# Performance work log

Hardware: AMD Instinct MI355X
Metric: run time of the kernel (lower is better)

Reference implementation:

```python
import jax, jax.numpy as jnp
import numpy as np

B, S, H = 2, 2048, 1024
E, K, F = 64, 8, 512
NORM_TOPK = True
CAP_FACTOR = 2.0


def setup_inputs() -> dict:
    key = jax.random.key(0)
    k0, k1, k2, k3, k4 = jax.random.split(key, 5)
    s_h = 1.0 / np.sqrt(H)
    s_f = 1.0 / np.sqrt(F)
    return {
        "hidden_states": jax.random.normal(k0, (B, S, H), jnp.float32),
        "w_gate": jax.random.normal(k1, (H, E), jnp.float32) * s_h,  # gate: Linear(H->E), no bias
        "w1": jax.random.normal(k2, (E, H, F), jnp.float32) * s_h,   # gate_proj per expert
        "w3": jax.random.normal(k3, (E, H, F), jnp.float32) * s_h,   # up_proj per expert
        "w2": jax.random.normal(k4, (E, F, H), jnp.float32) * s_f,   # down_proj per expert
    }


def reference(hidden_states, w_gate, w1, w3, w2):
    b, s, h = hidden_states.shape
    e = w_gate.shape[1]
    t = b * s
    x = hidden_states.reshape(t, h)
    router_logits = x @ w_gate                                   # [T, E]
    probs = jax.nn.softmax(router_logits.astype(jnp.float32), axis=-1)
    topw, sel = jax.lax.top_k(probs, K)                          # [T, K]
    if NORM_TOPK:
        topw = topw / jnp.sum(topw, axis=-1, keepdims=True)
    topw = topw.astype(x.dtype)

    a = t * K                                                    # total assignments
    c = int(CAP_FACTOR * a / e)                                  # static per-expert capacity
    sel_flat = sel.reshape(a)
    w_flat = topw.reshape(a)
    tok = jnp.repeat(jnp.arange(t), K)
    order = jnp.argsort(sel_flat, stable=True)                   # group assignments by expert
    e_s, t_s, w_s = sel_flat[order], tok[order], w_flat[order]
    counts = jnp.bincount(sel_flat, length=e)
    starts = jnp.cumsum(counts) - counts
    pos = jnp.arange(a) - starts[e_s]                            # position within expert group
    valid = pos < c
    slot = jnp.where(valid, e_s * c + pos, e * c)                # overflow -> dropped sentinel slot

    # dispatch: gather tokens into per-expert contiguous buffer [E, C, H]
    buf = jnp.zeros((e * c + 1, h), x.dtype).at[slot].set(x[t_s])
    xb = buf[: e * c].reshape(e, c, h)
    # grouped gated-SiLU MLP per expert
    g = jnp.einsum('ech,ehf->ecf', xb, w1)
    u = jnp.einsum('ech,ehf->ecf', xb, w3)
    yb = jnp.einsum('ecf,efh->ech', jax.nn.silu(g) * u, w2).reshape(e * c, h)
    # combine: weighted scatter-add back to tokens
    contrib = yb[jnp.minimum(slot, e * c - 1)] * (w_s * valid.astype(x.dtype))[:, None]
    out = jnp.zeros((t, h), x.dtype).at[t_s].add(contrib)
    return out.reshape(b, s, h), router_logits
```

## Files before the change

### kernel.cpp

```cpp
#include <hip/hip_runtime.h>
#include <hip/hip_bf16.h>

#define T_TOK 4096
#define H_DIM 1024
#define E_EXP 64
#define TOPK  8
#define F_DIM 512
#define CAP   1024
#define A_TOT (T_TOK * TOPK)

typedef _Float16 f16;
typedef _Float16 f16x4 __attribute__((ext_vector_type(4)));
typedef _Float16 f16x8 __attribute__((ext_vector_type(8)));
typedef float    f32x4 __attribute__((ext_vector_type(4)));

__global__ __launch_bounds__(256) void pack_all_kernel(
    const float* __restrict__ w1, const float* __restrict__ w3,
    const float* __restrict__ w2,
    f16* __restrict__ w1p, f16* __restrict__ w3p, f16* __restrict__ w2p)
{
    __shared__ f16 Ls[32][516];
    const int tid = threadIdx.x;
    const int bid = blockIdx.x;
    const float* src; f16* dst; int Nd, kb, e, kt, ch;
    if (bid < 2048)      { src = w1; dst = w1p; Nd = 512;  kb = 32; e = bid >> 5;          kt = bid & 31;          ch = 0; }
    else if (bid < 4096) { src = w3; dst = w3p; Nd = 512;  kb = 32; e = (bid - 2048) >> 5; kt = (bid - 2048) & 31; ch = 0; }
    else { src = w2; dst = w2p; Nd = 1024; kb = 16; int r = bid - 4096; e = r >> 5; kt = (r >> 1) & 15; ch = r & 1; }
    const int Kd = kb << 5;

    const float* base = src + ((size_t)e * Kd + kt * 32) * Nd + ch * 512;
    #pragma unroll
    for (int p = 0; p < 16; ++p) {
        int idx = p * 256 + tid;
        int row = idx >> 7, c4 = (idx & 127) * 4;
        float4 v = *(const float4*)(base + (size_t)row * Nd + c4);
        f16x4 hv;
        hv[0] = (f16)v.x; hv[1] = (f16)v.y; hv[2] = (f16)v.z; hv[3] = (f16)v.w;
        *(f16x4*)&Ls[row][c4] = hv;
    }
    __syncthreads();
    const int lane = tid & 63, wvi = tid >> 6;
    const int jj = lane & 15, qq = lane >> 4;
    const int ntb = Nd >> 4;
    #pragma unroll
    for (int i = 0; i < 8; ++i) {
        int ntl = wvi * 8 + i;
        f16x8 o;
        #pragma unroll
        for (int j = 0; j < 8; ++j)
            o[j] = Ls[qq * 8 + j][ntl * 16 + jj];
        int ntg = ch * 32 + ntl;
        size_t chunk = ((size_t)e * ntb + ntg) * kb + kt;
        *(f16x8*)(dst + chunk * 512 + lane * 8) = o;
    }
}

__global__ __launch_bounds__(256) void router_kernel(
    const float* __restrict__ x, const float* __restrict__ wg,
    float* __restrict__ logits_out, int* __restrict__ sel,
    float* __restrict__ wgtA, f16* __restrict__ xh)
{
    __shared__ float xs[16][128];
    __shared__ float ls[16][65];
    const int tid = threadIdx.x;
    const int e  = tid & 63;
    const int tg = tid >> 6;
    const int tb = blockIdx.x * 16;

    float acc[4] = {0.f, 0.f, 0.f, 0.f};
    for (int h0 = 0; h0 < H_DIM; h0 += 128) {
        {
            int r  = tid >> 4;
            int c0 = (tid & 15) * 8;
            const float4* src = (const float4*)(x + (size_t)(tb + r) * H_DIM + h0 + c0);
            float4 v0 = src[0], v1 = src[1];
            *(float4*)&xs[r][c0]     = v0;
            *(float4*)&xs[r][c0 + 4] = v1;
            f16x8 hv;
            hv[0] = (f16)v0.x; hv[1] = (f16)v0.y; hv[2] = (f16)v0.z; hv[3] = (f16)v0.w;
            hv[4] = (f16)v1.x; hv[5] = (f16)v1.y; hv[6] = (f16)v1.z; hv[7] = (f16)v1.w;
            *(f16x8*)(xh + (size_t)(tb + r) * H_DIM + h0 + c0) = hv;
        }
        __syncthreads();
        for (int hh = 0; hh < 128; ++hh) {
            float w = wg[(size_t)(h0 + hh) * E_EXP + e];
            #pragma unroll
            for (int i = 0; i < 4; ++i)
                acc[i] = fmaf(xs[tg * 4 + i][hh], w, acc[i]);
        }
        __syncthreads();
    }
    #pragma unroll
    for (int i = 0; i < 4; ++i) {
        int tt = tg * 4 + i;
        logits_out[(size_t)(tb + tt) * E_EXP + e] = acc[i];
        ls[tt][e] = acc[i];
    }
    __syncthreads();
    if (tid < 16) {
        int tt = tid;
        float lv[8]; int li[8];
        for (int k = 0; k < 8; ++k) {
            float m = -1e30f; int mi = 0;
            for (int j = 0; j < 64; ++j) {
                float v = ls[tt][j];
                if (v > m) { m = v; mi = j; }
            }
            lv[k] = m; li[k] = mi;
            ls[tt][mi] = -1e30f;
        }
        float s = 0.f, wv[8];
        for (int k = 0; k < 8; ++k) { wv[k] = __expf(lv[k] - lv[0]); s += wv[k]; }
        float inv = 1.f / s;
        for (int k = 0; k < 8; ++k) {
            int a = (tb + tt) * TOPK + k;
            sel[a]  = li[k];
            wgtA[a] = wv[k] * inv;
        }
    }
}

__global__ __launch_bounds__(256) void build_lists_kernel(
    const int* __restrict__ sel,
    int* __restrict__ tok_list, int* __restrict__ slotA,
    int* __restrict__ counts)
{
    __shared__ int sc[256];
    const int e = blockIdx.x;
    const int tid = threadIdx.x;
    const int per = A_TOT / 256;
    const int a0 = tid * per;
    int cnt = 0;
    for (int i = 0; i < per; ++i) cnt += (sel[a0 + i] == e) ? 1 : 0;
    sc[tid] = cnt;
    __syncthreads();
    for (int s = 1; s < 256; s <<= 1) {
        int v = (tid >= s) ? sc[tid - s] : 0;
        __syncthreads();
        sc[tid] += v;
        __syncthreads();
    }
    int total = sc[255];
    int pos = sc[tid] - cnt;
    if (tid == 0) counts[e] = (total < CAP) ? total : CAP;
    for (int i = 0; i < per; ++i) {
        int a = a0 + i;
        if (sel[a] == e) {
            if (pos < CAP) {
                tok_list[e * CAP + pos] = a >> 3;
                slotA[a] = e * CAP + pos;
            } else {
                slotA[a] = -1;
            }
            pos++;
        }
    }
}

#define MFMA16(a, b, c) __builtin_amdgcn_mfma_f32_16x16x32_f16(a, b, c, 0, 0, 0)

__global__ __launch_bounds__(256) void gemm1_kernel(
    const f16* __restrict__ xh, const f16* __restrict__ w1p,
    const f16* __restrict__ w3p, const int* __restrict__ tok_list,
    const int* __restrict__ counts, f16* __restrict__ P)
{
    const int id = blockIdx.x;
    const int x7 = id & 7, r = id >> 3;
    const int ft = r & 7, mt = (r >> 3) & 15, eh = r >> 7;
    const int e = x7 + 8 * eh;
    const int cnt = counts[e];
    const int m0 = mt * 64;
    if (m0 >= cnt) return;
    const int bf = ft * 64;

    __shared__ f16 Xs[2][64][64];
    __shared__ int tok_s[64];

    const int tid = threadIdx.x;
    const int lane = tid & 63, wv = tid >> 6;
    const int jj = lane & 15, qq = lane >> 4;
    const int sr = tid >> 3, sc = (tid & 7) * 8;
    const int swz_w = ((tid & 7) ^ (sr & 7)) * 8;
    const int x8 = jj & 7;
    const int s0 = (qq ^ x8) * 8;
    const int s1 = ((qq + 4) ^ x8) * 8;

    if (tid < 64) {
        int m = m0 + tid;
        tok_s[tid] = (m < cnt) ? tok_list[e * CAP + m] : tok_list[e * CAP];
    }
    __syncthreads();
    const size_t rowA = (size_t)tok_s[sr] * H_DIM + sc;
    const size_t rowB = (size_t)tok_s[sr + 32] * H_DIM + sc;

    const int nt = ft * 4 + wv;
    const f16* w1a = w1p + ((size_t)(e * 32 + nt) * 32) * 512 + lane * 8;
    const f16* w3a = w3p + ((size_t)(e * 32 + nt) * 32) * 512 + lane * 8;

    f32x4 accG[4], accU[4];
    #pragma unroll
    for (int i = 0; i < 4; ++i) {
        accG[i] = (f32x4){0.f, 0.f, 0.f, 0.f};
        accU[i] = (f32x4){0.f, 0.f, 0.f, 0.f};
    }

    {
        f16x8 a = *(const f16x8*)(xh + rowA);
        f16x8 b = *(const f16x8*)(xh + rowB);
        *(f16x8*)&Xs[0][sr][swz_w]      = a;
        *(f16x8*)&Xs[0][sr + 32][swz_w] = b;
    }
    f16x8 cG0 = *(const f16x8*)(w1a);
    f16x8 cG1 = *(const f16x8*)(w1a + 512);
    f16x8 cU0 = *(const f16x8*)(w3a);
    f16x8 cU1 = *(const f16x8*)(w3a + 512);

    #pragma unroll
    for (int it = 0; it < 16; ++it) {
        const int k0 = it * 64;
        __syncthreads();
        f16x8 xn0, xn1, nG0, nG1, nU0, nU1;
        if (it < 15) {
            xn0 = *(const f16x8*)(xh + rowA + k0 + 64);
            xn1 = *(const f16x8*)(xh + rowB + k0 + 64);
            size_t kg = (size_t)(2 * it + 2) * 512;
            nG0 = *(const f16x8*)(w1a + kg);
            nG1 = *(const f16x8*)(w1a + kg + 512);
            nU0 = *(const f16x8*)(w3a + kg);
            nU1 = *(const f16x8*)(w3a + kg + 512);
        }
        const int buf = it & 1;
        #pragma unroll
        for (int m2 = 0; m2 < 4; ++m2) {
            f16x8 a0 = *(const f16x8*)&Xs[buf][m2 * 16 + jj][s0];
            f16x8 a1 = *(const f16x8*)&Xs[buf][m2 * 16 + jj][s1];
            accG[m2] = MFMA16(a0, cG0, accG[m2]);
            accU[m2] = MFMA16(a0, cU0, accU[m2]);
            accG[m2] = MFMA16(a1, cG1, accG[m2]);
            accU[m2] = MFMA16(a1, cU1, accU[m2]);
        }
        if (it < 15) {
            *(f16x8*)&Xs[buf ^ 1][sr][swz_w]      = xn0;
            *(f16x8*)&Xs[buf ^ 1][sr + 32][swz_w] = xn1;
            cG0 = nG0; cG1 = nG1; cU0 = nU0; cU1 = nU1;
        }
    }
    #pragma unroll
    for (int m2 = 0; m2 < 4; ++m2) {
        #pragma unroll
        for (int rr = 0; rr < 4; ++rr) {
            int row = m2 * 16 + qq * 4 + rr;
            float gg = accG[m2][rr], u = accU[m2][rr];
            float p = gg / (1.f + __expf(-gg)) * u;
            P[(size_t)(e * CAP + m0 + row) * F_DIM + bf + wv * 16 + jj] = (f16)p;
        }
    }
}

__global__ __launch_bounds__(256) void gemm2_kernel(
    const f16* __restrict__ P, const f16* __restrict__ w2p,
    const int* __restrict__ counts, f16* __restrict__ Y)
{
    const int id = blockIdx.x;
    const int x7 = id & 7, r = id >> 3;
    const int ht = r & 7, mt = (r >> 3) & 15, eh = r >> 7;
    const int e = x7 + 8 * eh;
    const int cnt = counts[e];
    const int m0 = mt * 64;
    if (m0 >= cnt) return;
    const int h0 = ht * 128;

    __shared__ f16 Ps[2][64][64];

    const int tid = threadIdx.x;
    const int lane = tid & 63, wv = tid >> 6;
    const int jj = lane & 15, qq = lane >> 4;
    const int sr = tid >> 3, sc = (tid & 7) * 8;
    const int swz_w = ((tid & 7) ^ (sr & 7)) * 8;
    const int x8 = jj & 7;
    const int s0 = (qq ^ x8) * 8;
    const int s1 = ((qq + 4) ^ x8) * 8;

    const size_t pbase = (size_t)(e * CAP + m0) * F_DIM;
    const f16* wA = w2p + ((size_t)(e * 64 + ht * 8 + wv) * 16) * 512 + lane * 8;
    const f16* wB = w2p + ((size_t)(e * 64 + ht * 8 + wv + 4) * 16) * 512 + lane * 8;

    f32x4 accA[4], accB[4];
    #pragma unroll
    for (int i = 0; i < 4; ++i) {
        accA[i] = (f32x4){0.f, 0.f, 0.f, 0.f};
        accB[i] = (f32x4){0.f, 0.f, 0.f, 0.f};
    }

    {
        f16x8 a = *(const f16x8*)(P + pbase + (size_t)sr * F_DIM + sc);
        f16x8 b = *(const f16x8*)(P + pbase + (size_t)(sr + 32) * F_DIM + sc);
        *(f16x8*)&Ps[0][sr][swz_w]      = a;
        *(f16x8*)&Ps[0][sr + 32][swz_w] = b;
    }
    f16x8 cA0 = *(const f16x8*)(wA);
    f16x8 cA1 = *(const f16x8*)(wA + 512);
    f16x8 cB0 = *(const f16x8*)(wB);
    f16x8 cB1 = *(const f16x8*)(wB + 512);

    #pragma unroll
    for (int it = 0; it < 8; ++it) {
        const int k0 = it * 64;
        __syncthreads();
        f16x8 pn0, pn1, nA0, nA1, nB0, nB1;
        if (it < 7) {
            pn0 = *(const f16x8*)(P + pbase + (size_t)sr * F_DIM + k0 + 64 + sc);
            pn1 = *(const f16x8*)(P + pbase + (size_t)(sr + 32) * F_DIM + k0 + 64 + sc);
            size_t kg = (size_t)(2 * it + 2) * 512;
            nA0 = *(const f16x8*)(wA + kg);
            nA1 = *(const f16x8*)(wA + kg + 512);
            nB0 = *(const f16x8*)(wB + kg);
            nB1 = *(const f16x8*)(wB + kg + 512);
        }
        const int buf = it & 1;
        #pragma unroll
        for (int m2 = 0; m2 < 4; ++m2) {
            f16x8 a0 = *(const f16x8*)&Ps[buf][m2 * 16 + jj][s0];
            f16x8 a1 = *(const f16x8*)&Ps[buf][m2 * 16 + jj][s1];
            accA[m2] = MFMA16(a0, cA0, accA[m2]);
            accB[m2] = MFMA16(a0, cB0, accB[m2]);
            accA[m2] = MFMA16(a1, cA1, accA[m2]);
            accB[m2] = MFMA16(a1, cB1, accB[m2]);
        }
        if (it < 7) {
            *(f16x8*)&Ps[buf ^ 1][sr][swz_w]      = pn0;
            *(f16x8*)&Ps[buf ^ 1][sr + 32][swz_w] = pn1;
            cA0 = nA0; cA1 = nA1; cB0 = nB0; cB1 = nB1;
        }
    }
    f16* yb = Y + (size_t)(e * CAP + m0) * H_DIM + h0 + wv * 16 + jj;
    #pragma unroll
    for (int m2 = 0; m2 < 4; ++m2) {
        #pragma unroll
        for (int rr = 0; rr < 4; ++rr) {
            int row = m2 * 16 + qq * 4 + rr;
            yb[(size_t)row * H_DIM]      = (f16)accA[m2][rr];
            yb[(size_t)row * H_DIM + 64] = (f16)accB[m2][rr];
        }
    }
}

__global__ __launch_bounds__(256) void combine_kernel(
    const f16* __restrict__ Y, const int* __restrict__ slotA,
    const float* __restrict__ wgtA, float* __restrict__ out)
{
    const int tid = threadIdx.x;
    const int t  = blockIdx.x * 2 + (tid >> 7);
    const int hc = (tid & 127) * 8;
    float acc[8] = {0.f, 0.f, 0.f, 0.f, 0.f, 0.f, 0.f, 0.f};
    const int base = t * TOPK;
    #pragma unroll
    for (int k = 0; k < 8; ++k) {
        int s   = slotA[base + k];
        float w = wgtA[base + k];
        if (s >= 0) {
            f16x8 y = *(const f16x8*)(Y + (size_t)s * H_DIM + hc);
            #pragma unroll
            for (int j = 0; j < 8; ++j) acc[j] += w * (float)y[j];
        }
    }
    float4 o0 = {acc[0], acc[1], acc[2], acc[3]};
    float4 o1 = {acc[4], acc[5], acc[6], acc[7]};
    *(float4*)(out + (size_t)t * H_DIM + hc)     = o0;
    *(float4*)(out + (size_t)t * H_DIM + hc + 4) = o1;
}

extern "C" void kernel_launch(void* const* d_in, const int* in_sizes, int n_in,
                              void* d_out, int out_size, void* d_ws, size_t ws_size,
                              hipStream_t stream) {
    const float* x  = (const float*)d_in[0];
    const float* wg = (const float*)d_in[1];
    const float* w1 = (const float*)d_in[2];
    const float* w3 = (const float*)d_in[3];
    const float* w2 = (const float*)d_in[4];

    float* out    = (float*)d_out;
    float* logits = out + (size_t)T_TOK * H_DIM;

    char* ws = (char*)d_ws;
    int*   sel      = (int*)  (ws);
    float* wgtA     = (float*)(ws + (128 << 10));
    int*   tok_list = (int*)  (ws + (256 << 10));
    int*   slotA    = (int*)  (ws + (512 << 10));
    int*   counts   = (int*)  (ws + (768 << 10));
    f16*   xh       = (f16*)  (ws + (size_t)(1 << 20));
    f16*   P        = (f16*)  (ws + (size_t)(9 << 20));
    f16*   w1p      = (f16*)  (ws + (size_t)(73 << 20));
    f16*   w3p      = (f16*)  (ws + (size_t)(137 << 20));
    f16*   w2p      = (f16*)  (ws + (size_t)(201 << 20));
    f16*   Y        = (f16*)  (ws + (size_t)(73 << 20));

    pack_all_kernel<<<6144, 256, 0, stream>>>(w1, w3, w2, w1p, w3p, w2p);
    router_kernel<<<T_TOK / 16, 256, 0, stream>>>(x, wg, logits, sel, wgtA, xh);
    build_lists_kernel<<<E_EXP, 256, 0, stream>>>(sel, tok_list, slotA, counts);
    gemm1_kernel<<<8192, 256, 0, stream>>>(xh, w1p, w3p, tok_list, counts, P);
    gemm2_kernel<<<8192, 256, 0, stream>>>(P, w2p, counts, Y);
    combine_kernel<<<T_TOK / 2, 256, 0, stream>>>(Y, slotA, wgtA, out);
}
```

Measured before the change: 662.3 us.

## Reorder packed expert weights k-major and stage GEMM outputs through LDS

The packed expert weight chunks are reordered so that chunks for adjacent N-tiles at the same K step sit next to each other in memory. Concurrently running waves and blocks therefore read nearby addresses in both GEMM kernels. The gated-SiLU output P and the down-projection output Y are now written to shared memory first and then stored to global memory as 16-byte vectors per row. This replaces the earlier scattered 2-byte stores and costs two extra barriers plus an LDS round trip per block.

```diff
diff --git a/kernel.cpp b/kernel.cpp
--- a/kernel.cpp
+++ b/kernel.cpp
@@ -22,10 +22,10 @@
     __shared__ f16 Ls[32][516];
     const int tid = threadIdx.x;
     const int bid = blockIdx.x;
-    const float* src; f16* dst; int Nd, kb, e, kt, ch;
-    if (bid < 2048)      { src = w1; dst = w1p; Nd = 512;  kb = 32; e = bid >> 5;          kt = bid & 31;          ch = 0; }
-    else if (bid < 4096) { src = w3; dst = w3p; Nd = 512;  kb = 32; e = (bid - 2048) >> 5; kt = (bid - 2048) & 31; ch = 0; }
-    else { src = w2; dst = w2p; Nd = 1024; kb = 16; int r = bid - 4096; e = r >> 5; kt = (r >> 1) & 15; ch = r & 1; }
+    const float* src; f16* dst; int Nd, kb, ntb, e, kt, ch;
+    if (bid < 2048)      { src = w1; dst = w1p; Nd = 512;  kb = 32; ntb = 32; e = bid >> 5;          kt = bid & 31;          ch = 0; }
+    else if (bid < 4096) { src = w3; dst = w3p; Nd = 512;  kb = 32; ntb = 32; e = (bid - 2048) >> 5; kt = (bid - 2048) & 31; ch = 0; }
+    else { src = w2; dst = w2p; Nd = 1024; kb = 16; ntb = 64; int r = bid - 4096; e = r >> 5; kt = (r >> 1) & 15; ch = r & 1; }
     const int Kd = kb << 5;
 
     const float* base = src + ((size_t)e * Kd + kt * 32) * Nd + ch * 512;
@@ -41,7 +41,6 @@
     __syncthreads();
     const int lane = tid & 63, wvi = tid >> 6;
     const int jj = lane & 15, qq = lane >> 4;
-    const int ntb = Nd >> 4;
     #pragma unroll
     for (int i = 0; i < 8; ++i) {
         int ntl = wvi * 8 + i;
@@ -49,8 +48,7 @@
         #pragma unroll
         for (int j = 0; j < 8; ++j)
             o[j] = Ls[qq * 8 + j][ntl * 16 + jj];
-        int ntg = ch * 32 + ntl;
-        size_t chunk = ((size_t)e * ntb + ntg) * kb + kt;
+        size_t chunk = ((size_t)e * kb + kt) * ntb + (ch * 32 + ntl);
         *(f16x8*)(dst + chunk * 512 + lane * 8) = o;
     }
 }
@@ -194,8 +192,9 @@
     const size_t rowB = (size_t)tok_s[sr + 32] * H_DIM + sc;
 
     const int nt = ft * 4 + wv;
-    const f16* w1a = w1p + ((size_t)(e * 32 + nt) * 32) * 512 + lane * 8;
-    const f16* w3a = w3p + ((size_t)(e * 32 + nt) * 32) * 512 + lane * 8;
+    const f16* w1a = w1p + ((size_t)(e * 32) * 32 + nt) * 512 + lane * 8;
+    const f16* w3a = w3p + ((size_t)(e * 32) * 32 + nt) * 512 + lane * 8;
+    const size_t KH = (size_t)32 * 512;
 
     f32x4 accG[4], accU[4];
     #pragma unroll
@@ -211,9 +210,9 @@
         *(f16x8*)&Xs[0][sr + 32][swz_w] = b;
     }
     f16x8 cG0 = *(const f16x8*)(w1a);
-    f16x8 cG1 = *(const f16x8*)(w1a + 512);
+    f16x8 cG1 = *(const f16x8*)(w1a + KH);
     f16x8 cU0 = *(const f16x8*)(w3a);
-    f16x8 cU1 = *(const f16x8*)(w3a + 512);
+    f16x8 cU1 = *(const f16x8*)(w3a + KH);
 
     #pragma unroll
     for (int it = 0; it < 16; ++it) {
@@ -223,11 +222,11 @@
         if (it < 15) {
             xn0 = *(const f16x8*)(xh + rowA + k0 + 64);
             xn1 = *(const f16x8*)(xh + rowB + k0 + 64);
-            size_t kg = (size_t)(2 * it + 2) * 512;
+            size_t kg = (size_t)(2 * it + 2) * KH;
             nG0 = *(const f16x8*)(w1a + kg);
-            nG1 = *(const f16x8*)(w1a + kg + 512);
+            nG1 = *(const f16x8*)(w1a + kg + KH);
             nU0 = *(const f16x8*)(w3a + kg);
-            nU1 = *(const f16x8*)(w3a + kg + 512);
+            nU1 = *(const f16x8*)(w3a + kg + KH);
         }
         const int buf = it & 1;
         #pragma unroll
@@ -245,6 +244,8 @@
             cG0 = nG0; cG1 = nG1; cU0 = nU0; cU1 = nU1;
         }
     }
+    __syncthreads();
+    f16 (*Ct)[72] = (f16(*)[72])Xs;
     #pragma unroll
     for (int m2 = 0; m2 < 4; ++m2) {
         #pragma unroll
@@ -252,8 +253,16 @@
             int row = m2 * 16 + qq * 4 + rr;
             float gg = accG[m2][rr], u = accU[m2][rr];
             float p = gg / (1.f + __expf(-gg)) * u;
-            P[(size_t)(e * CAP + m0 + row) * F_DIM + bf + wv * 16 + jj] = (f16)p;
-        }
+            Ct[row][wv * 16 + jj] = (f16)p;
+        }
+    }
+    __syncthreads();
+    #pragma unroll
+    for (int i = 0; i < 2; ++i) {
+        int row = (tid >> 3) + i * 32;
+        int col = (tid & 7) * 8;
+        f16x8 v = *(f16x8*)&Ct[row][col];
+        *(f16x8*)(P + (size_t)(e * CAP + m0 + row) * F_DIM + bf + col) = v;
     }
 }
 
@@ -282,8 +291,9 @@
     const int s1 = ((qq + 4) ^ x8) * 8;
 
     const size_t pbase = (size_t)(e * CAP + m0) * F_DIM;
-    const f16* wA = w2p + ((size_t)(e * 64 + ht * 8 + wv) * 16) * 512 + lane * 8;
-    const f16* wB = w2p + ((size_t)(e * 64 + ht * 8 + wv + 4) * 16) * 512 + lane * 8;
+    const size_t KH = (size_t)64 * 512;
+    const f16* wA = w2p + ((size_t)(e * 16) * 64 + ht * 8 + wv) * 512 + lane * 8;
+    const f16* wB = wA + (size_t)4 * 512;
 
     f32x4 accA[4], accB[4];
     #pragma unroll
@@ -299,9 +309,9 @@
         *(f16x8*)&Ps[0][sr + 32][swz_w] = b;
     }
     f16x8 cA0 = *(const f16x8*)(wA);
-    f16x8 cA1 = *(const f16x8*)(wA + 512);
+    f16x8 cA1 = *(const f16x8*)(wA + KH);
     f16x8 cB0 = *(const f16x8*)(wB);
-    f16x8 cB1 = *(const f16x8*)(wB + 512);
+    f16x8 cB1 = *(const f16x8*)(wB + KH);
 
     #pragma unroll
     for (int it = 0; it < 8; ++it) {
@@ -311,11 +321,11 @@
         if (it < 7) {
             pn0 = *(const f16x8*)(P + pbase + (size_t)sr * F_DIM + k0 + 64 + sc);
             pn1 = *(const f16x8*)(P + pbase + (size_t)(sr + 32) * F_DIM + k0 + 64 + sc);
-            size_t kg = (size_t)(2 * it + 2) * 512;
+            size_t kg = (size_t)(2 * it + 2) * KH;
             nA0 = *(const f16x8*)(wA + kg);
-            nA1 = *(const f16x8*)(wA + kg + 512);
+            nA1 = *(const f16x8*)(wA + kg + KH);
             nB0 = *(const f16x8*)(wB + kg);
-            nB1 = *(const f16x8*)(wB + kg + 512);
+            nB1 = *(const f16x8*)(wB + kg + KH);
         }
         const int buf = it & 1;
         #pragma unroll
@@ -333,15 +343,24 @@
             cA0 = nA0; cA1 = nA1; cB0 = nB0; cB1 = nB1;
         }
     }
-    f16* yb = Y + (size_t)(e * CAP + m0) * H_DIM + h0 + wv * 16 + jj;
+    __syncthreads();
+    f16 (*Ct2)[128] = (f16(*)[128])Ps;
     #pragma unroll
     for (int m2 = 0; m2 < 4; ++m2) {
         #pragma unroll
         for (int rr = 0; rr < 4; ++rr) {
             int row = m2 * 16 + qq * 4 + rr;
-            yb[(size_t)row * H_DIM]      = (f16)accA[m2][rr];
-            yb[(size_t)row * H_DIM + 64] = (f16)accB[m2][rr];
-        }
+            Ct2[row][wv * 16 + jj]      = (f16)accA[m2][rr];
+            Ct2[row][wv * 16 + jj + 64] = (f16)accB[m2][rr];
+        }
+    }
+    __syncthreads();
+    #pragma unroll
+    for (int i = 0; i < 4; ++i) {
+        int row = (tid >> 4) + i * 16;
+        int col = (tid & 15) * 8;
+        f16x8 v = *(f16x8*)&Ct2[row][col];
+        *(f16x8*)(Y + (size_t)(e * CAP + m0 + row) * H_DIM + h0 + col) = v;
     }
 }
 
```

After: 679.4 us. +2.6%, slower.
